# Optimization experiments

Hardware: AMD Instinct MI355X
Metric: run time of the kernel (lower is better)

Reference implementation:

```python
import jax, jax.numpy as jnp
from jax import lax
import numpy as np

S, B, T, N, FJ, H, MF, M = 8, 64, 64, 16, 32, 128, 16, 8
NN = S + M  # total machine-graph nodes
EPS = 1e-5
SLOPE = 0.2


def layernorm(x, g, b):
    mu = x.mean(-1, keepdims=True)
    var = ((x - mu) ** 2).mean(-1, keepdims=True)
    return (x - mu) / jnp.sqrt(var + EPS) * g + b


def gat(adj, x, W, a):
    # dense GAT layer: x [..., N, Fin], adj [..., N, N]
    h = x @ W  # [..., N, O]
    O = W.shape[1]
    f1 = h @ a[:O]  # [..., N]
    f2 = h @ a[O:]
    e = jax.nn.leaky_relu(f1[..., :, None] + f2[..., None, :], SLOPE)
    e = jnp.where(adj > 0, e, jnp.float32(-1e9))
    return jax.nn.softmax(e, axis=-1) @ h


def job_enc(adj, x, Ws, As):
    t = jnp.tanh(gat(adj, x, Ws[0], As[0]))
    t = jnp.tanh(gat(adj, t, Ws[1], As[1]) + t)
    t = jnp.tanh(gat(adj, t, Ws[2], As[2]) + t)
    t = jnp.tanh(t + gat(adj, t, Ws[3], As[3]))
    return t.mean(-2)  # mean over ops dim


def lstm_last(x, Wih, Whh, b):
    # x: [Bx, T, H]; returns final hidden state [Bx, H]
    xs = jnp.einsum('bti,gi->tbg', x, Wih) + b  # [T, Bx, 4H]
    h0 = jnp.zeros((x.shape[0], Whh.shape[1]), x.dtype)

    def step(carry, xt):
        h, c = carry
        g = xt + h @ Whh.T
        i, f, gg, o = jnp.split(g, 4, axis=-1)
        c = jax.nn.sigmoid(f) * c + jax.nn.sigmoid(i) * jnp.tanh(gg)
        h = jax.nn.sigmoid(o) * jnp.tanh(c)
        return (h, c), None

    (h, _), _ = lax.scan(step, (h0, h0), xs)
    return h


def setup_inputs() -> dict:
    key = jax.random.key(0)
    ks = jax.random.split(key, 32)

    def adj(k, shape):
        a = jax.random.bernoulli(k, 0.4, shape).astype(jnp.int32)
        return jnp.maximum(a, jnp.eye(shape[-1], dtype=jnp.int32))

    mfeat = jax.random.normal(ks[4], (B, NN, MF), jnp.float32)
    # stage nodes (first S) have feature[...,0] > 0; machine nodes < 0
    mfeat = mfeat.at[:, :S, 0].set(jnp.abs(mfeat[:, :S, 0]) + 0.1)
    mfeat = mfeat.at[:, S:, 0].set(-jnp.abs(mfeat[:, S:, 0]) - 0.1)

    sc = 0.08
    inp = {
        'j_stages_f': jax.random.normal(ks[0], (S, B, T, N, FJ), jnp.float32),
        'j_stages_a': adj(ks[1], (S, B, T, N, N)),
        'j_machine_f': jax.random.normal(ks[2], (B, M, N, FJ), jnp.float32),
        'j_machine_a': adj(ks[3], (B, M, N, N)),
        'machine_f': mfeat,
        'machine_a': adj(ks[5], (B, NN, NN)),
        'jg1_W': jax.random.normal(ks[6], (FJ, H), jnp.float32) * sc,
        'jgW': jax.random.normal(ks[7], (3, H, H), jnp.float32) * sc,
        'jga': jax.random.normal(ks[8], (4, 2 * H), jnp.float32) * sc,
        'lstm_Wih': jax.random.normal(ks[9], (4 * H, H), jnp.float32) * sc,
        'lstm_Whh': jax.random.normal(ks[10], (4 * H, H), jnp.float32) * sc,
        'lstm_b': jnp.zeros((4 * H,), jnp.float32),
        'mfe_W': jax.random.normal(ks[11], (MF, H), jnp.float32) * sc,
        'mfe_b': jnp.zeros((H,), jnp.float32),
        'n2_g': jnp.ones((H,), jnp.float32),
        'n2_b': jnp.zeros((H,), jnp.float32),
        'me_W': jax.random.normal(ks[12], (2 * H, H), jnp.float32) * sc,
        'me_b': jnp.zeros((H,), jnp.float32),
        'n3_g': jnp.ones((H,), jnp.float32),
        'n3_b': jnp.zeros((H,), jnp.float32),
        'mgW': jax.random.normal(ks[13], (4, H, H), jnp.float32) * sc,
        'mga': jax.random.normal(ks[14], (4, 2 * H), jnp.float32) * sc,
        'mng': jnp.ones((4, H), jnp.float32),
        'mnb': jnp.zeros((4, H), jnp.float32),
    }
    return inp


def reference(j_stages_f, j_stages_a, j_machine_f, j_machine_a, machine_f,
              machine_a, jg1_W, jgW, jga, lstm_Wih, lstm_Whh, lstm_b,
              mfe_W, mfe_b, n2_g, n2_b, me_W, me_b, n3_g, n3_b,
              mgW, mga, mng, mnb):
    Ws = [jg1_W, jgW[0], jgW[1], jgW[2]]
    As = [jga[0], jga[1], jga[2], jga[3]]

    # per-stage job encoding + LSTM over job sequence
    stage_emb = jax.vmap(lambda a, f: job_enc(a, f, Ws, As))(j_stages_a, j_stages_f)  # [S,B,T,H]
    hlast = lstm_last(stage_emb.reshape(S * B, T, H), lstm_Wih, lstm_Whh, lstm_b)
    j_encoded = hlast.reshape(S, B, H).transpose(1, 0, 2)  # [B,S,H]

    # machine-side job graph encoding (shared encoder)
    jm = job_enc(j_machine_a, j_machine_f, Ws, As)  # [B,M,H]

    # machine node embedding
    mfh = jnp.tanh(layernorm(machine_f @ mfe_W + mfe_b, n2_g, n2_b))  # [B,NN,H]

    # static routing: first S nodes -> stage contexts, rest -> machine contexts
    ctx = jnp.concatenate([j_encoded, jm], axis=1)  # [B,NN,H]
    nodes = jnp.concatenate([mfh, ctx], axis=-1)  # [B,NN,2H]
    nodes = jnp.tanh(layernorm(nodes @ me_W + me_b, n3_g, n3_b))

    h = nodes
    prev = None
    for k in range(4):
        h2 = layernorm(gat(machine_a, h, mgW[k], mga[k]), mng[k], mnb[k])
        if k != 0:
            h2 = h2 + prev
        h = jnp.tanh(h2)
        prev = h
    return h.mean(axis=1)  # [B, H]
```

## Files before the change

kernel.cpp:

```cpp
#include <hip/hip_runtime.h>
#include <hip/hip_bf16.h>
#include <math.h>

#define S_ 8
#define B_ 64
#define T_ 64
#define N_ 16
#define FJ_ 32
#define H_ 128
#define MF_ 16
#define M_ 8
#define SB_ 512
#define G1_ 32768
#define G2_ 512

#define CPAD 132
#define PPAD 17

typedef short bf16x8 __attribute__((ext_vector_type(8)));
typedef short bf16x4 __attribute__((ext_vector_type(4)));
typedef float f32x4 __attribute__((ext_vector_type(4)));
typedef unsigned short u16;

__device__ __forceinline__ u16 f2bf(float f) {
  union { float f; unsigned u; } v; v.f = f;
  unsigned r = v.u + 0x7FFFu + ((v.u >> 16) & 1u);
  return (u16)(r >> 16);
}
__device__ __forceinline__ unsigned pk2(float lo, float hi) {
  __hip_bfloat162 h2 = __float22bfloat162_rn(make_float2(lo, hi));
  union { __hip_bfloat162 h; unsigned u; } x; x.h = h2; return x.u;
}
__device__ __forceinline__ bf16x4 mkfrag(unsigned a, unsigned b) {
  union { bf16x4 v; unsigned u[2]; } x; x.u[0] = a; x.u[1] = b; return x.v;
}
__device__ __forceinline__ f32x4 mfma16(bf16x4 a, bf16x4 b, f32x4 c) {
#if __has_builtin(__builtin_amdgcn_mfma_f32_16x16x16bf16_1k)
  return __builtin_amdgcn_mfma_f32_16x16x16bf16_1k(a, b, c, 0, 0, 0);
#else
  asm("v_mfma_f32_16x16x16_bf16 %0, %1, %2, %0" : "+v"(c) : "v"(a), "v"(b));
  return c;
#endif
}
__device__ __forceinline__ float frcp(float x) {
#if __has_builtin(__builtin_amdgcn_rcpf)
  return __builtin_amdgcn_rcpf(x);
#else
  return 1.f / x;
#endif
}
__device__ __forceinline__ float frsq(float x) {
#if __has_builtin(__builtin_amdgcn_rsqf)
  return __builtin_amdgcn_rsqf(x);
#else
  return rsqrtf(x);
#endif
}
__device__ __forceinline__ float ftanh(float x) {
  float e = __expf(2.f * x);
  return fmaf(-2.f, frcp(e + 1.f), 1.f);
}
__device__ __forceinline__ float sigmoidf_(float x) {
  return frcp(1.f + __expf(-x));
}

__device__ __forceinline__ void fma8(float (&acc)[8], float xv, float4 wa, float4 wb) {
  acc[0] = fmaf(xv, wa.x, acc[0]); acc[1] = fmaf(xv, wa.y, acc[1]);
  acc[2] = fmaf(xv, wa.z, acc[2]); acc[3] = fmaf(xv, wa.w, acc[3]);
  acc[4] = fmaf(xv, wb.x, acc[4]); acc[5] = fmaf(xv, wb.y, acc[5]);
  acc[6] = fmaf(xv, wb.z, acc[6]); acc[7] = fmaf(xv, wb.w, acc[7]);
}
__device__ __forceinline__ float grp16_sum(float v) {
#pragma unroll
  for (int m = 1; m < 16; m <<= 1) v += __shfl_xor(v, m);
  return v;
}
__device__ __forceinline__ float grp16_max(float v) {
#pragma unroll
  for (int m = 1; m < 16; m <<= 1) v = fmaxf(v, __shfl_xor(v, m));
  return v;
}
__device__ __forceinline__ void ln_row(float (&v)[8], const float* gw, const float* bw, int j0) {
  float s1 = 0.f, s2 = 0.f;
#pragma unroll
  for (int c = 0; c < 8; ++c) { s1 += v[c]; s2 += v[c] * v[c]; }
  s1 = grp16_sum(s1); s2 = grp16_sum(s2);
  float mu = s1 * (1.f / 128.f);
  float var = s2 * (1.f / 128.f) - mu * mu;
  float rstd = frsq(var + 1e-5f);
#pragma unroll
  for (int c = 0; c < 8; ++c) v[c] = (v[c] - mu) * rstd * gw[j0 + c] + bw[j0 + c];
}

__global__ __launch_bounds__(256) void pack_w_kernel(
    const float* __restrict__ W0, const float* __restrict__ W123,
    const float* __restrict__ jga,
    const float* __restrict__ Wih, const float* __restrict__ Whh,
    u16* __restrict__ wpk0, u16* __restrict__ wpkL,
    u16* __restrict__ wpkIH, u16* __restrict__ wpkHH)
{
  int idx = blockIdx.x * 256 + threadIdx.x;
  if (idx < 4608) {
    int e = idx & 3, l = (idx >> 2) & 63, t = idx >> 8;
    int n = t >> 1, kk = t & 1;
    int q = l >> 4, cc = l & 15;
    int k = 16 * kk + 4 * q + e;
    float v = 0.f;
    if (n < 8) v = W0[k * 128 + 16 * n + cc];
    else if (cc < 2) {
      const float* a = jga + cc * 128;
      float s = 0.f;
      for (int j = 0; j < 128; ++j) s += W0[k * 128 + j] * a[j];
      v = s;
    }
    wpk0[idx] = f2bf(v);
  } else if (idx < 59904) {
    int id = idx - 4608;
    int e = id & 3, l = (id >> 2) & 63;
    int t2 = id >> 8;
    int t = t2 % 72, layer = t2 / 72;
    int n = t >> 3, kk = t & 7;
    int q = l >> 4, cc = l & 15;
    int k = 16 * kk + 4 * q + e;
    const float* W = W123 + (size_t)layer * 16384;
    float v = 0.f;
    if (n < 8) v = W[k * 128 + 16 * n + cc];
    else if (cc < 2) {
      const float* a = jga + (layer + 1) * 256 + cc * 128;
      float s = 0.f;
      for (int j = 0; j < 128; ++j) s += W[k * 128 + j] * a[j];
      v = s;
    }
    wpkL[id] = f2bf(v);
  } else if (idx < 125440) {
    int id = idx - 59904;
    int e = id & 7, l = (id >> 3) & 63, kk = (id >> 9) & 3, n = id >> 11;
    int gate = 16 * n + (l & 15), k = 32 * kk + 8 * (l >> 4) + e;
    wpkIH[id] = f2bf(Wih[gate * 128 + k]);
  } else if (idx < 190976) {
    int id = idx - 125440;
    int e = id & 7, l = (id >> 3) & 63, kk = (id >> 9) & 3, n = id >> 11;
    int gate = 16 * n + (l & 15), k = 32 * kk + 8 * (l >> 4) + e;
    wpkHH[id] = f2bf(Whh[gate * 128 + k]);
  }
}

__global__ __launch_bounds__(512) __attribute__((amdgpu_waves_per_eu(2, 4)))
void gat_mfma_kernel(
    const float* __restrict__ xinA,
    const int* __restrict__ adjA,
    float* __restrict__ outmA, u16* __restrict__ outbfA,
    const float* __restrict__ xinB,
    const int* __restrict__ adjB,
    float* __restrict__ outmB, u16* __restrict__ outbfB,
    const u16* __restrict__ wpk0, const u16* __restrict__ wpkL)
{
  __shared__ __align__(16) u16 wbuf[18432];
  __shared__ __align__(16) float fbuf[8][32];

  const int wv = threadIdx.x >> 6;
  const int l = threadIdx.x & 63;
  const int c = l & 15, q = l >> 4;
  float* fb = fbuf[wv];

  const float* xin; const int* adjin; float* outm; u16* outbf; int g;
  if (blockIdx.x < G1_ / 8) {
    xin = xinA; adjin = adjA; outm = outmA; outbf = outbfA;
    g = blockIdx.x * 8 + wv;
  } else {
    xin = xinB; adjin = adjB; outm = outmB; outbf = outbfB;
    g = (blockIdx.x - G1_ / 8) * 8 + wv;
  }

  auto stage = [&](const u16* src, int nbytes) {
    const float4* s4 = (const float4*)src;
    float4* d4 = (float4*)wbuf;
    int n16 = nbytes >> 4;
    for (int i = threadIdx.x; i < n16; i += 512) d4[i] = s4[i];
  };

  int4 A1 = *(const int4*)(adjin + (size_t)g * 256 + c * 16 + 4 * q);

  f32x4 res[8];
  bf16x4 hfrag[8];

  auto softmax_pv = [&](f32x4 Cf, bool resid) {
    if (c < 2) *(f32x4*)(fb + c * 16 + 4 * q) = Cf;
    float f1v = fb[c];
    float4 f2v = *(const float4*)(fb + 16 + 4 * q);
    float ev[4] = {f1v + f2v.x, f1v + f2v.y, f1v + f2v.z, f1v + f2v.w};
#pragma unroll
    for (int e = 0; e < 4; ++e) ev[e] = (ev[e] >= 0.f) ? ev[e] : 0.2f * ev[e];
    ev[0] = (A1.x > 0) ? ev[0] : -1e9f;
    ev[1] = (A1.y > 0) ? ev[1] : -1e9f;
    ev[2] = (A1.z > 0) ? ev[2] : -1e9f;
    ev[3] = (A1.w > 0) ? ev[3] : -1e9f;
    float mx = fmaxf(fmaxf(ev[0], ev[1]), fmaxf(ev[2], ev[3]));
    mx = fmaxf(mx, __shfl_xor(mx, 16));
    mx = fmaxf(mx, __shfl_xor(mx, 32));
    float sm = 0.f;
#pragma unroll
    for (int e = 0; e < 4; ++e) { ev[e] = __expf(ev[e] - mx); sm += ev[e]; }
    sm += __shfl_xor(sm, 16);
    sm += __shfl_xor(sm, 32);
    float zinv = frcp(sm);
    bf16x4 pfrag = mkfrag(pk2(ev[0] * zinv, ev[1] * zinv), pk2(ev[2] * zinv, ev[3] * zinv));
#pragma unroll
    for (int m = 0; m < 8; ++m) {
      f32x4 o = resid ? res[m] : (f32x4){0.f, 0.f, 0.f, 0.f};
      o = mfma16(hfrag[m], pfrag, o);
      f32x4 t;
      t[0] = ftanh(o[0]); t[1] = ftanh(o[1]); t[2] = ftanh(o[2]); t[3] = ftanh(o[3]);
      res[m] = t;
    }
  };

  stage(wpk0, 9216);
  __syncthreads();
  {
    bf16x4 xf[2];
    const float* xg = xin + (size_t)g * 512 + c * 32 + 4 * q;
    float4 x1 = *(const float4*)xg;
    float4 x2 = *(const float4*)(xg + 16);
    xf[0] = mkfrag(pk2(x1.x, x1.y), pk2(x1.z, x1.w));
    xf[1] = mkfrag(pk2(x2.x, x2.y), pk2(x2.z, x2.w));
#pragma unroll
    for (int n = 0; n < 8; ++n) {
      f32x4 Ch = (f32x4){0.f, 0.f, 0.f, 0.f};
#pragma unroll
      for (int kk = 0; kk < 2; ++kk) {
        bf16x4 wf = *(const bf16x4*)(wbuf + ((n * 2 + kk) * 64 + l) * 4);
        Ch = mfma16(xf[kk], wf, Ch);
      }
      hfrag[n] = mkfrag(pk2(Ch[0], Ch[1]), pk2(Ch[2], Ch[3]));
    }
    f32x4 Cf = (f32x4){0.f, 0.f, 0.f, 0.f};
#pragma unroll
    for (int kk = 0; kk < 2; ++kk) {
      bf16x4 wf = *(const bf16x4*)(wbuf + ((16 + kk) * 64 + l) * 4);
      Cf = mfma16(xf[kk], wf, Cf);
    }
    softmax_pv(Cf, false);
  }
  __syncthreads();

#pragma unroll 1
  for (int layer = 1; layer < 4; ++layer) {
    stage(wpkL + (size_t)(layer - 1) * 18432, 36864);
    __syncthreads();
    bf16x4 xf[8];
#pragma unroll
    for (int kk = 0; kk < 8; ++kk)
      xf[kk] = mkfrag(pk2(res[kk][0], res[kk][1]), pk2(res[kk][2], res[kk][3]));
#pragma unroll
    for (int n = 0; n < 8; ++n) {
      f32x4 Ch = (f32x4){0.f, 0.f, 0.f, 0.f};
#pragma unroll
      for (int kk = 0; kk < 8; ++kk) {
        bf16x4 wf = *(const bf16x4*)(wbuf + ((n * 8 + kk) * 64 + l) * 4);
        Ch = mfma16(xf[kk], wf, Ch);
      }
      hfrag[n] = mkfrag(pk2(Ch[0], Ch[1]), pk2(Ch[2], Ch[3]));
    }
    f32x4 Cf = (f32x4){0.f, 0.f, 0.f, 0.f};
#pragma unroll
    for (int kk = 0; kk < 8; ++kk) {
      bf16x4 wf = *(const bf16x4*)(wbuf + ((64 + kk) * 64 + l) * 4);
      Cf = mfma16(xf[kk], wf, Cf);
    }
    softmax_pv(Cf, true);
    __syncthreads();
  }

  u16* tb = wbuf + wv * 2176;
#pragma unroll
  for (int m = 0; m < 8; ++m) {
    uint2 u;
    u.x = pk2(res[m][0], res[m][1]);
    u.y = pk2(res[m][2], res[m][3]);
    *(uint2*)(tb + c * 136 + 16 * m + 4 * q) = u;
  }
  {
    float s0 = 0.f, s1 = 0.f;
#pragma unroll
    for (int node = 0; node < 16; ++node) {
      unsigned u = *(const unsigned*)(tb + node * 136 + 2 * l);
      union { unsigned u; float f; } lo, hi;
      lo.u = u << 16; hi.u = u & 0xffff0000u;
      s0 += lo.f; s1 += hi.f;
    }
    s0 *= 0.0625f; s1 *= 0.0625f;
    *(float2*)(outm + (size_t)g * 128 + 2 * l) = make_float2(s0, s1);
    *(unsigned*)(outbf + (size_t)g * 128 + 2 * l) = pk2(s0, s1);
  }
}

__global__ __launch_bounds__(512) __attribute__((amdgpu_waves_per_eu(1, 2)))
void lstm_fused_kernel(
    const u16* __restrict__ emb_bf,
    const u16* __restrict__ wpkIH, const u16* __restrict__ wpkHH,
    const float* __restrict__ bvec,
    float* __restrict__ hlast)
{
  __shared__ unsigned hbuf[2][1024];
  const int tid = threadIdx.x;
  const int w = tid >> 6, l = tid & 63;
  const int c = l & 15, q = l >> 4;
  const int seq0 = blockIdx.x * 16;
  const int swz = (c & 7) << 2;

  bf16x8 aih[4][4], ahh[4][4];
#pragma unroll
  for (int m = 0; m < 4; ++m)
#pragma unroll
    for (int kk = 0; kk < 4; ++kk) {
      int n = 8 * m + w;
      aih[m][kk] = *(const bf16x8*)(wpkIH + ((size_t)((n * 4 + kk) * 64 + l)) * 8);
      ahh[m][kk] = *(const bf16x8*)(wpkHH + ((size_t)((n * 4 + kk) * 64 + l)) * 8);
    }
  float bias[4][4];
#pragma unroll
  for (int m = 0; m < 4; ++m)
#pragma unroll
    for (int r = 0; r < 4; ++r) bias[m][r] = bvec[128 * m + 16 * w + 4 * q + r];

  hbuf[0][tid] = 0u;
  hbuf[0][512 + tid] = 0u;
  __syncthreads();

  const u16* xbase = emb_bf + ((size_t)(seq0 + c)) * 64 * 128 + q * 8;

  f32x4 accih[4];
  {
    bf16x8 xf[4];
#pragma unroll
    for (int kk = 0; kk < 4; ++kk) xf[kk] = *(const bf16x8*)(xbase + kk * 32);
#pragma unroll
    for (int m = 0; m < 4; ++m) {
      f32x4 a = (f32x4){0.f, 0.f, 0.f, 0.f};
#pragma unroll
      for (int kk = 0; kk < 4; ++kk)
        a = __builtin_amdgcn_mfma_f32_16x16x32_bf16(aih[m][kk], xf[kk], a, 0, 0, 0);
      accih[m] = a;
    }
  }

  float cst[4] = {0.f, 0.f, 0.f, 0.f};
  float hv[4] = {0.f, 0.f, 0.f, 0.f};
  int pb = 0;
#pragma unroll 1
  for (int t = 0; t < T_; ++t) {
    bf16x8 hf[4];
#pragma unroll
    for (int kk = 0; kk < 4; ++kk) {
      int j0 = (16 * kk + 4 * q) ^ swz;
      hf[kk] = *(const bf16x8*)&hbuf[pb][c * 64 + j0];
    }
    f32x4 acc[4];
#pragma unroll
    for (int m = 0; m < 4; ++m) {
      f32x4 a = accih[m];
#pragma unroll
      for (int kk = 0; kk < 4; ++kk)
        a = __builtin_amdgcn_mfma_f32_16x16x32_bf16(ahh[m][kk], hf[kk], a, 0, 0, 0);
      acc[m] = a;
    }
#pragma unroll
    for (int r = 0; r < 4; ++r) {
      float ig = acc[0][r] + bias[0][r];
      float fg = acc[1][r] + bias[1][r];
      float gg = acc[2][r] + bias[2][r];
      float og = acc[3][r] + bias[3][r];
      cst[r] = sigmoidf_(fg) * cst[r] + sigmoidf_(ig) * ftanh(gg);
      hv[r] = sigmoidf_(og) * ftanh(cst[r]);
    }
    {
      int j0 = (8 * w + 2 * q) ^ swz;
      uint2 u2; u2.x = pk2(hv[0], hv[1]); u2.y = pk2(hv[2], hv[3]);
      *(uint2*)&hbuf[pb ^ 1][c * 64 + j0] = u2;
    }
    __syncthreads();
    pb ^= 1;
    if (t < T_ - 1) {
      bf16x8 xf[4];
      const u16* xr = xbase + (t + 1) * 128;
#pragma unroll
      for (int kk = 0; kk < 4; ++kk) xf[kk] = *(const bf16x8*)(xr + kk * 32);
#pragma unroll
      for (int m = 0; m < 4; ++m) {
        f32x4 a = (f32x4){0.f, 0.f, 0.f, 0.f};
#pragma unroll
        for (int kk = 0; kk < 4; ++kk)
          a = __builtin_amdgcn_mfma_f32_16x16x32_bf16(aih[m][kk], xf[kk], a, 0, 0, 0);
        accih[m] = a;
      }
    }
  }
#pragma unroll
  for (int r = 0; r < 4; ++r)
    hlast[((size_t)(seq0 + c)) * 128 + 16 * w + 4 * q + r] = hv[r];
}

__global__ __launch_bounds__(256) __attribute__((amdgpu_waves_per_eu(2, 4)))
void machine_kernel(
    const float* __restrict__ machine_f, const int* __restrict__ machine_a,
    const float* __restrict__ hlast, const float* __restrict__ jm,
    const float* __restrict__ mfe_W, const float* __restrict__ mfe_b,
    const float* __restrict__ n2_g, const float* __restrict__ n2_b,
    const float* __restrict__ me_W, const float* __restrict__ me_b,
    const float* __restrict__ n3_g, const float* __restrict__ n3_b,
    const float* __restrict__ mgW, const float* __restrict__ mga,
    const float* __restrict__ mng, const float* __restrict__ mnb,
    float* __restrict__ outp)
{
  __shared__ float mf[256];
  __shared__ int adjs[256];
  __shared__ __align__(16) float ctx[16 * CPAD];
  __shared__ __align__(16) float mfh[16 * CPAD];
  __shared__ __align__(16) float cur[16 * CPAD];
  __shared__ __align__(16) float tmp[16 * CPAD];
  __shared__ __align__(16) float prevb[16 * CPAD];
  __shared__ float pm[16 * PPAD];
  __shared__ float f1s[16], f2s[16];

  const int b = blockIdx.x;
  const int tid = threadIdx.x;
  const int i = tid >> 4;
  const int jb = tid & 15;
  const int j0 = jb << 3;

  mf[tid] = machine_f[(size_t)b * 256 + tid];
  adjs[tid] = machine_a[(size_t)b * 256 + tid];
  {
    const float* src = (i < 8) ? (hlast + ((size_t)i * B_ + b) * H_)
                               : (jm + ((size_t)b * M_ + (i - 8)) * H_);
    *(float4*)(ctx + i * CPAD + j0) = ((const float4*)src)[jb * 2];
    *(float4*)(ctx + i * CPAD + j0 + 4) = ((const float4*)src)[jb * 2 + 1];
  }
  __syncthreads();

  {
    float acc[8];
#pragma unroll
    for (int c = 0; c < 8; ++c) acc[c] = 0.f;
#pragma unroll
    for (int k = 0; k < MF_; ++k) {
      float xv = mf[i * 16 + k];
      float4 wa = *(const float4*)(mfe_W + (size_t)k * H_ + j0);
      float4 wb = *(const float4*)(mfe_W + (size_t)k * H_ + j0 + 4);
      fma8(acc, xv, wa, wb);
    }
#pragma unroll
    for (int c = 0; c < 8; ++c) acc[c] += mfe_b[j0 + c];
    ln_row(acc, n2_g, n2_b, j0);
#pragma unroll
    for (int c = 0; c < 8; ++c) mfh[i * CPAD + j0 + c] = ftanh(acc[c]);
  }
  __syncthreads();

  {
    float acc[8];
#pragma unroll
    for (int c = 0; c < 8; ++c) acc[c] = 0.f;
#pragma unroll 4
    for (int k = 0; k < H_; ++k) {
      float xv = mfh[i * CPAD + k];
      float4 wa = *(const float4*)(me_W + (size_t)k * H_ + j0);
      float4 wb = *(const float4*)(me_W + (size_t)k * H_ + j0 + 4);
      fma8(acc, xv, wa, wb);
    }
#pragma unroll 4
    for (int k = 0; k < H_; ++k) {
      float xv = ctx[i * CPAD + k];
      float4 wa = *(const float4*)(me_W + (size_t)(128 + k) * H_ + j0);
      float4 wb = *(const float4*)(me_W + (size_t)(128 + k) * H_ + j0 + 4);
      fma8(acc, xv, wa, wb);
    }
#pragma unroll
    for (int c = 0; c < 8; ++c) acc[c] += me_b[j0 + c];
    ln_row(acc, n3_g, n3_b, j0);
#pragma unroll
    for (int c = 0; c < 8; ++c) cur[i * CPAD + j0 + c] = ftanh(acc[c]);
  }
  __syncthreads();

  for (int l = 0; l < 4; ++l) {
    const float* W = mgW + (size_t)l * H_ * H_;
    const float* a0 = mga + l * 256;
    const float* a1 = a0 + 128;

    float acc[8];
#pragma unroll
    for (int c = 0; c < 8; ++c) acc[c] = 0.f;
#pragma unroll 4
    for (int k = 0; k < H_; ++k) {
      float xv = cur[i * CPAD + k];
      float4 wa = *(const float4*)(W + (size_t)k * H_ + j0);
      float4 wb = *(const float4*)(W + (size_t)k * H_ + j0 + 4);
      fma8(acc, xv, wa, wb);
    }
    *(float4*)(tmp + i * CPAD + j0) = make_float4(acc[0], acc[1], acc[2], acc[3]);
    *(float4*)(tmp + i * CPAD + j0 + 4) = make_float4(acc[4], acc[5], acc[6], acc[7]);

    float p1 = 0.f, p2 = 0.f;
#pragma unroll
    for (int c = 0; c < 8; ++c) {
      p1 = fmaf(acc[c], a0[j0 + c], p1);
      p2 = fmaf(acc[c], a1[j0 + c], p2);
    }
    p1 = grp16_sum(p1); p2 = grp16_sum(p2);
    if (jb == 0) { f1s[i] = p1; f2s[i] = p2; }
    __syncthreads();

    {
      int jc = jb;
      float e = f1s[i] + f2s[jc];
      e = (e >= 0.f) ? e : 0.2f * e;
      if (adjs[i * 16 + jc] <= 0) e = -1e9f;
      float mxv = grp16_max(e);
      float ex = __expf(e - mxv);
      float smv = grp16_sum(ex);
      pm[i * PPAD + jc] = ex * frcp(smv);
    }
    __syncthreads();

    float o[8];
#pragma unroll
    for (int c = 0; c < 8; ++c) o[c] = 0.f;
#pragma unroll
    for (int k = 0; k < 16; ++k) {
      float pv = pm[i * PPAD + k];
      float4 ha = *(const float4*)(tmp + k * CPAD + j0);
      float4 hb = *(const float4*)(tmp + k * CPAD + j0 + 4);
      fma8(o, pv, ha, hb);
    }
    ln_row(o, mng + l * H_, mnb + l * H_, j0);
#pragma unroll
    for (int c = 0; c < 8; ++c) {
      float v = o[c] + ((l > 0) ? prevb[i * CPAD + j0 + c] : 0.f);
      v = ftanh(v);
      cur[i * CPAD + j0 + c] = v;
      prevb[i * CPAD + j0 + c] = v;
    }
    __syncthreads();
  }

  if (tid < 128) {
    float s = 0.f;
#pragma unroll
    for (int r = 0; r < 16; ++r) s += cur[r * CPAD + tid];
    outp[(size_t)b * H_ + tid] = s * (1.f / 16.f);
  }
}

extern "C" void kernel_launch(void* const* d_in, const int* in_sizes, int n_in,
                              void* d_out, int out_size, void* d_ws, size_t ws_size,
                              hipStream_t stream) {
  const float* j_stages_f  = (const float*)d_in[0];
  const int*   j_stages_a  = (const int*)d_in[1];
  const float* j_machine_f = (const float*)d_in[2];
  const int*   j_machine_a = (const int*)d_in[3];
  const float* machine_f   = (const float*)d_in[4];
  const int*   machine_a   = (const int*)d_in[5];
  const float* jg1_W       = (const float*)d_in[6];
  const float* jgW         = (const float*)d_in[7];
  const float* jga         = (const float*)d_in[8];
  const float* lstm_Wih    = (const float*)d_in[9];
  const float* lstm_Whh    = (const float*)d_in[10];
  const float* lstm_b      = (const float*)d_in[11];
  const float* mfe_W       = (const float*)d_in[12];
  const float* mfe_b       = (const float*)d_in[13];
  const float* n2_g        = (const float*)d_in[14];
  const float* n2_b        = (const float*)d_in[15];
  const float* me_W        = (const float*)d_in[16];
  const float* me_b        = (const float*)d_in[17];
  const float* n3_g        = (const float*)d_in[18];
  const float* n3_b        = (const float*)d_in[19];
  const float* mgW         = (const float*)d_in[20];
  const float* mga         = (const float*)d_in[21];
  const float* mng         = (const float*)d_in[22];
  const float* mnb         = (const float*)d_in[23];
  float* out = (float*)d_out;

  char* ws = (char*)d_ws;
  u16*   emb_bf  = (u16*)ws;
  u16*   jmbf    = (u16*)(ws + 8388608);
  float* jm      = (float*)(ws + 8519680);
  float* hlast   = (float*)(ws + 8781824);
  float* outm_s  = (float*)(ws + 9043968);
  u16*   wpk0    = (u16*)(ws + 25821184);
  u16*   wpkL    = (u16*)(ws + 25830400);
  u16*   wpkIH   = (u16*)(ws + 25940992);
  u16*   wpkHH   = (u16*)(ws + 26072064);

  pack_w_kernel<<<746, 256, 0, stream>>>(jg1_W, jgW, jga, lstm_Wih, lstm_Whh,
                                         wpk0, wpkL, wpkIH, wpkHH);
  gat_mfma_kernel<<<G1_ / 8 + G2_ / 8, 512, 0, stream>>>(
      j_stages_f, j_stages_a, outm_s, emb_bf,
      j_machine_f, j_machine_a, jm, jmbf, wpk0, wpkL);
  lstm_fused_kernel<<<SB_ / 16, 512, 0, stream>>>(emb_bf, wpkIH, wpkHH, lstm_b, hlast);
  machine_kernel<<<B_, 256, 0, stream>>>(machine_f, machine_a, hlast, jm,
                                         mfe_W, mfe_b, n2_g, n2_b, me_W, me_b,
                                         n3_g, n3_b, mgW, mga, mng, mnb, out);
}
```

Before: 368.6 us.

## Use 16x16x32 MFMA in GAT, halve LSTM sequences per block, prefetch inputs

The GAT kernel moves from 16x16x16 bf16 MFMA to 16x16x32 MFMA. The weight packing is rebuilt to match, and the fragments are reshuffled with cross-lane shuffles, including zero-padding the attention matrix for the K=16 P·V product. The unused float stage output write is dropped. The LSTM kernel now handles 8 sequences per block instead of 16, doubling the block count, and computes the next step's input projection before the barrier while prefetching the input two steps ahead. These changes aim to use fewer MFMA instructions and to add parallelism and latency hiding to the serial LSTM. The cost is extra shuffles and wasted half tiles in the LSTM MFMAs.

```diff
diff --git a/kernel.cpp b/kernel.cpp
--- a/kernel.cpp
+++ b/kernel.cpp
@@ -18,7 +18,6 @@
 #define PPAD 17
 
 typedef short bf16x8 __attribute__((ext_vector_type(8)));
-typedef short bf16x4 __attribute__((ext_vector_type(4)));
 typedef float f32x4 __attribute__((ext_vector_type(4)));
 typedef unsigned short u16;
 
@@ -31,16 +30,12 @@
   __hip_bfloat162 h2 = __float22bfloat162_rn(make_float2(lo, hi));
   union { __hip_bfloat162 h; unsigned u; } x; x.h = h2; return x.u;
 }
-__device__ __forceinline__ bf16x4 mkfrag(unsigned a, unsigned b) {
-  union { bf16x4 v; unsigned u[2]; } x; x.u[0] = a; x.u[1] = b; return x.v;
-}
-__device__ __forceinline__ f32x4 mfma16(bf16x4 a, bf16x4 b, f32x4 c) {
-#if __has_builtin(__builtin_amdgcn_mfma_f32_16x16x16bf16_1k)
-  return __builtin_amdgcn_mfma_f32_16x16x16bf16_1k(a, b, c, 0, 0, 0);
-#else
-  asm("v_mfma_f32_16x16x16_bf16 %0, %1, %2, %0" : "+v"(c) : "v"(a), "v"(b));
-  return c;
-#endif
+__device__ __forceinline__ bf16x8 mk8(unsigned a, unsigned b, unsigned cc, unsigned d) {
+  union { bf16x8 v; unsigned u[4]; } x;
+  x.u[0] = a; x.u[1] = b; x.u[2] = cc; x.u[3] = d; return x.v;
+}
+__device__ __forceinline__ f32x4 mfma32(bf16x8 a, bf16x8 b, f32x4 c) {
+  return __builtin_amdgcn_mfma_f32_16x16x32_bf16(a, b, c, 0, 0, 0);
 }
 __device__ __forceinline__ float frcp(float x) {
 #if __has_builtin(__builtin_amdgcn_rcpf)
@@ -101,10 +96,9 @@
 {
   int idx = blockIdx.x * 256 + threadIdx.x;
   if (idx < 4608) {
-    int e = idx & 3, l = (idx >> 2) & 63, t = idx >> 8;
-    int n = t >> 1, kk = t & 1;
+    int e = idx & 7, l = (idx >> 3) & 63, n = idx >> 9;
     int q = l >> 4, cc = l & 15;
-    int k = 16 * kk + 4 * q + e;
+    int k = 8 * q + e;
     float v = 0.f;
     if (n < 8) v = W0[k * 128 + 16 * n + cc];
     else if (cc < 2) {
@@ -116,12 +110,12 @@
     wpk0[idx] = f2bf(v);
   } else if (idx < 59904) {
     int id = idx - 4608;
-    int e = id & 3, l = (id >> 2) & 63;
-    int t2 = id >> 8;
-    int t = t2 % 72, layer = t2 / 72;
-    int n = t >> 3, kk = t & 7;
+    int e = id & 7, l = (id >> 3) & 63;
+    int t2 = id >> 9;
+    int t = t2 % 36, layer = t2 / 36;
+    int n = t >> 2, kk = t & 3;
     int q = l >> 4, cc = l & 15;
-    int k = 16 * kk + 4 * q + e;
+    int k = 32 * kk + 8 * q + e;
     const float* W = W123 + (size_t)layer * 16384;
     float v = 0.f;
     if (n < 8) v = W[k * 128 + 16 * n + cc];
@@ -147,11 +141,9 @@
 
 __global__ __launch_bounds__(512) __attribute__((amdgpu_waves_per_eu(2, 4)))
 void gat_mfma_kernel(
-    const float* __restrict__ xinA,
-    const int* __restrict__ adjA,
+    const float* __restrict__ xinA, const int* __restrict__ adjA,
     float* __restrict__ outmA, u16* __restrict__ outbfA,
-    const float* __restrict__ xinB,
-    const int* __restrict__ adjB,
+    const float* __restrict__ xinB, const int* __restrict__ adjB,
     float* __restrict__ outmB, u16* __restrict__ outbfB,
     const u16* __restrict__ wpk0, const u16* __restrict__ wpkL)
 {
@@ -182,7 +174,12 @@
   int4 A1 = *(const int4*)(adjin + (size_t)g * 256 + c * 16 + 4 * q);
 
   f32x4 res[8];
-  bf16x4 hfrag[8];
+  unsigned hp0[8], hp1[8];
+  const int sLo = c + 16 * (2 * q);
+  const int sHi = sLo + 16;
+  const int sA = c + 16 * (2 * (q & 1));
+  const int sB = sA + 16;
+  const bool qhi = (q >= 2);
 
   auto softmax_pv = [&](f32x4 Cf, bool resid) {
     if (c < 2) *(f32x4*)(fb + c * 16 + 4 * q) = Cf;
@@ -204,42 +201,39 @@
     sm += __shfl_xor(sm, 16);
     sm += __shfl_xor(sm, 32);
     float zinv = frcp(sm);
-    bf16x4 pfrag = mkfrag(pk2(ev[0] * zinv, ev[1] * zinv), pk2(ev[2] * zinv, ev[3] * zinv));
-#pragma unroll
-    for (int m = 0; m < 8; ++m) {
-      f32x4 o = resid ? res[m] : (f32x4){0.f, 0.f, 0.f, 0.f};
-      o = mfma16(hfrag[m], pfrag, o);
+    unsigned pp0 = pk2(ev[0] * zinv, ev[1] * zinv);
+    unsigned pp1 = pk2(ev[2] * zinv, ev[3] * zinv);
+    unsigned w0 = __shfl(pp0, sLo), w1 = __shfl(pp1, sLo);
+    unsigned w2 = __shfl(pp0, sHi), w3 = __shfl(pp1, sHi);
+    if (qhi) { w0 = 0u; w1 = 0u; w2 = 0u; w3 = 0u; }
+    bf16x8 pfrag = mk8(w0, w1, w2, w3);
+#pragma unroll
+    for (int n = 0; n < 8; ++n) {
+      unsigned v0 = __shfl(hp0[n], sLo), v1 = __shfl(hp1[n], sLo);
+      unsigned v2 = __shfl(hp0[n], sHi), v3 = __shfl(hp1[n], sHi);
+      f32x4 o = resid ? res[n] : (f32x4){0.f, 0.f, 0.f, 0.f};
+      o = mfma32(mk8(v0, v1, v2, v3), pfrag, o);
       f32x4 t;
       t[0] = ftanh(o[0]); t[1] = ftanh(o[1]); t[2] = ftanh(o[2]); t[3] = ftanh(o[3]);
-      res[m] = t;
+      res[n] = t;
     }
   };
 
   stage(wpk0, 9216);
   __syncthreads();
   {
-    bf16x4 xf[2];
-    const float* xg = xin + (size_t)g * 512 + c * 32 + 4 * q;
+    const float* xg = xin + (size_t)g * 512 + c * 32 + q * 8;
     float4 x1 = *(const float4*)xg;
-    float4 x2 = *(const float4*)(xg + 16);
-    xf[0] = mkfrag(pk2(x1.x, x1.y), pk2(x1.z, x1.w));
-    xf[1] = mkfrag(pk2(x2.x, x2.y), pk2(x2.z, x2.w));
+    float4 x2 = *(const float4*)(xg + 4);
+    bf16x8 xf8 = mk8(pk2(x1.x, x1.y), pk2(x1.z, x1.w), pk2(x2.x, x2.y), pk2(x2.z, x2.w));
 #pragma unroll
     for (int n = 0; n < 8; ++n) {
       f32x4 Ch = (f32x4){0.f, 0.f, 0.f, 0.f};
-#pragma unroll
-      for (int kk = 0; kk < 2; ++kk) {
-        bf16x4 wf = *(const bf16x4*)(wbuf + ((n * 2 + kk) * 64 + l) * 4);
-        Ch = mfma16(xf[kk], wf, Ch);
-      }
-      hfrag[n] = mkfrag(pk2(Ch[0], Ch[1]), pk2(Ch[2], Ch[3]));
+      Ch = mfma32(xf8, *(const bf16x8*)(wbuf + (n * 64 + l) * 8), Ch);
+      hp0[n] = pk2(Ch[0], Ch[1]); hp1[n] = pk2(Ch[2], Ch[3]);
     }
     f32x4 Cf = (f32x4){0.f, 0.f, 0.f, 0.f};
-#pragma unroll
-    for (int kk = 0; kk < 2; ++kk) {
-      bf16x4 wf = *(const bf16x4*)(wbuf + ((16 + kk) * 64 + l) * 4);
-      Cf = mfma16(xf[kk], wf, Cf);
-    }
+    Cf = mfma32(xf8, *(const bf16x8*)(wbuf + (8 * 64 + l) * 8), Cf);
     softmax_pv(Cf, false);
   }
   __syncthreads();
@@ -248,26 +242,33 @@
   for (int layer = 1; layer < 4; ++layer) {
     stage(wpkL + (size_t)(layer - 1) * 18432, 36864);
     __syncthreads();
-    bf16x4 xf[8];
-#pragma unroll
-    for (int kk = 0; kk < 8; ++kk)
-      xf[kk] = mkfrag(pk2(res[kk][0], res[kk][1]), pk2(res[kk][2], res[kk][3]));
+    unsigned p0[8], p1[8];
+#pragma unroll
+    for (int m = 0; m < 8; ++m) {
+      p0[m] = pk2(res[m][0], res[m][1]);
+      p1[m] = pk2(res[m][2], res[m][3]);
+    }
+    bf16x8 xf[4];
+#pragma unroll
+    for (int kk = 0; kk < 4; ++kk) {
+      unsigned a0 = __shfl(p0[2 * kk], sA), b0 = __shfl(p0[2 * kk + 1], sA);
+      unsigned a1 = __shfl(p1[2 * kk], sA), b1 = __shfl(p1[2 * kk + 1], sA);
+      unsigned a2 = __shfl(p0[2 * kk], sB), b2 = __shfl(p0[2 * kk + 1], sB);
+      unsigned a3 = __shfl(p1[2 * kk], sB), b3 = __shfl(p1[2 * kk + 1], sB);
+      xf[kk] = mk8(qhi ? b0 : a0, qhi ? b1 : a1, qhi ? b2 : a2, qhi ? b3 : a3);
+    }
 #pragma unroll
     for (int n = 0; n < 8; ++n) {
       f32x4 Ch = (f32x4){0.f, 0.f, 0.f, 0.f};
 #pragma unroll
-      for (int kk = 0; kk < 8; ++kk) {
-        bf16x4 wf = *(const bf16x4*)(wbuf + ((n * 8 + kk) * 64 + l) * 4);
-        Ch = mfma16(xf[kk], wf, Ch);
-      }
-      hfrag[n] = mkfrag(pk2(Ch[0], Ch[1]), pk2(Ch[2], Ch[3]));
+      for (int kk = 0; kk < 4; ++kk)
+        Ch = mfma32(xf[kk], *(const bf16x8*)(wbuf + ((n * 4 + kk) * 64 + l) * 8), Ch);
+      hp0[n] = pk2(Ch[0], Ch[1]); hp1[n] = pk2(Ch[2], Ch[3]);
     }
     f32x4 Cf = (f32x4){0.f, 0.f, 0.f, 0.f};
 #pragma unroll
-    for (int kk = 0; kk < 8; ++kk) {
-      bf16x4 wf = *(const bf16x4*)(wbuf + ((64 + kk) * 64 + l) * 4);
-      Cf = mfma16(xf[kk], wf, Cf);
-    }
+    for (int kk = 0; kk < 4; ++kk)
+      Cf = mfma32(xf[kk], *(const bf16x8*)(wbuf + ((32 + kk) * 64 + l) * 8), Cf);
     softmax_pv(Cf, true);
     __syncthreads();
   }
@@ -290,7 +291,7 @@
       s0 += lo.f; s1 += hi.f;
     }
     s0 *= 0.0625f; s1 *= 0.0625f;
-    *(float2*)(outm + (size_t)g * 128 + 2 * l) = make_float2(s0, s1);
+    if (outm) *(float2*)(outm + (size_t)g * 128 + 2 * l) = make_float2(s0, s1);
     *(unsigned*)(outbf + (size_t)g * 128 + 2 * l) = pk2(s0, s1);
   }
 }
@@ -306,7 +307,8 @@
   const int tid = threadIdx.x;
   const int w = tid >> 6, l = tid & 63;
   const int c = l & 15, q = l >> 4;
-  const int seq0 = blockIdx.x * 16;
+  const int ce = c & 7;
+  const int seq0 = blockIdx.x * 8;
   const int swz = (c & 7) << 2;
 
   bf16x8 aih[4][4], ahh[4][4];
@@ -328,8 +330,9 @@
   hbuf[0][512 + tid] = 0u;
   __syncthreads();
 
-  const u16* xbase = emb_bf + ((size_t)(seq0 + c)) * 64 * 128 + q * 8;
-
+  const u16* xbase = emb_bf + ((size_t)(seq0 + ce)) * 64 * 128 + q * 8;
+
+  bf16x8 xnxt[4];
   f32x4 accih[4];
   {
     bf16x8 xf[4];
@@ -343,6 +346,8 @@
         a = __builtin_amdgcn_mfma_f32_16x16x32_bf16(aih[m][kk], xf[kk], a, 0, 0, 0);
       accih[m] = a;
     }
+#pragma unroll
+    for (int kk = 0; kk < 4; ++kk) xnxt[kk] = *(const bf16x8*)(xbase + 128 + kk * 32);
   }
 
   float cst[4] = {0.f, 0.f, 0.f, 0.f};
@@ -379,26 +384,29 @@
       uint2 u2; u2.x = pk2(hv[0], hv[1]); u2.y = pk2(hv[2], hv[3]);
       *(uint2*)&hbuf[pb ^ 1][c * 64 + j0] = u2;
     }
+    if (t < T_ - 1) {
+#pragma unroll
+      for (int m = 0; m < 4; ++m) {
+        f32x4 a = (f32x4){0.f, 0.f, 0.f, 0.f};
+#pragma unroll
+        for (int kk = 0; kk < 4; ++kk)
+          a = __builtin_amdgcn_mfma_f32_16x16x32_bf16(aih[m][kk], xnxt[kk], a, 0, 0, 0);
+        accih[m] = a;
+      }
+      if (t < T_ - 2) {
+        const u16* xr = xbase + (size_t)(t + 2) * 128;
+#pragma unroll
+        for (int kk = 0; kk < 4; ++kk) xnxt[kk] = *(const bf16x8*)(xr + kk * 32);
+      }
+    }
     __syncthreads();
     pb ^= 1;
-    if (t < T_ - 1) {
-      bf16x8 xf[4];
-      const u16* xr = xbase + (t + 1) * 128;
-#pragma unroll
-      for (int kk = 0; kk < 4; ++kk) xf[kk] = *(const bf16x8*)(xr + kk * 32);
-#pragma unroll
-      for (int m = 0; m < 4; ++m) {
-        f32x4 a = (f32x4){0.f, 0.f, 0.f, 0.f};
-#pragma unroll
-        for (int kk = 0; kk < 4; ++kk)
-          a = __builtin_amdgcn_mfma_f32_16x16x32_bf16(aih[m][kk], xf[kk], a, 0, 0, 0);
-        accih[m] = a;
-      }
-    }
-  }
-#pragma unroll
-  for (int r = 0; r < 4; ++r)
-    hlast[((size_t)(seq0 + c)) * 128 + 16 * w + 4 * q + r] = hv[r];
+  }
+  if (c < 8) {
+#pragma unroll
+    for (int r = 0; r < 4; ++r)
+      hlast[((size_t)(seq0 + ce)) * 128 + 16 * w + 4 * q + r] = hv[r];
+  }
 }
 
 __global__ __launch_bounds__(256) __attribute__((amdgpu_waves_per_eu(2, 4)))
@@ -484,9 +492,9 @@
   }
   __syncthreads();
 
-  for (int l = 0; l < 4; ++l) {
-    const float* W = mgW + (size_t)l * H_ * H_;
-    const float* a0 = mga + l * 256;
+  for (int ll = 0; ll < 4; ++ll) {
+    const float* W = mgW + (size_t)ll * H_ * H_;
+    const float* a0 = mga + ll * 256;
     const float* a1 = a0 + 128;
 
     float acc[8];
@@ -534,10 +542,10 @@
       float4 hb = *(const float4*)(tmp + k * CPAD + j0 + 4);
       fma8(o, pv, ha, hb);
     }
-    ln_row(o, mng + l * H_, mnb + l * H_, j0);
+    ln_row(o, mng + ll * H_, mnb + ll * H_, j0);
 #pragma unroll
     for (int c = 0; c < 8; ++c) {
-      float v = o[c] + ((l > 0) ? prevb[i * CPAD + j0 + c] : 0.f);
+      float v = o[c] + ((ll > 0) ? prevb[i * CPAD + j0 + c] : 0.f);
       v = ftanh(v);
       cur[i * CPAD + j0 + c] = v;
       prevb[i * CPAD + j0 + c] = v;
@@ -587,18 +595,17 @@
   u16*   jmbf    = (u16*)(ws + 8388608);
   float* jm      = (float*)(ws + 8519680);
   float* hlast   = (float*)(ws + 8781824);
-  float* outm_s  = (float*)(ws + 9043968);
-  u16*   wpk0    = (u16*)(ws + 25821184);
-  u16*   wpkL    = (u16*)(ws + 25830400);
-  u16*   wpkIH   = (u16*)(ws + 25940992);
-  u16*   wpkHH   = (u16*)(ws + 26072064);
+  u16*   wpk0    = (u16*)(ws + 9043968);
+  u16*   wpkL    = (u16*)(ws + 9053184);
+  u16*   wpkIH   = (u16*)(ws + 9163776);
+  u16*   wpkHH   = (u16*)(ws + 9294848);
 
   pack_w_kernel<<<746, 256, 0, stream>>>(jg1_W, jgW, jga, lstm_Wih, lstm_Whh,
                                          wpk0, wpkL, wpkIH, wpkHH);
   gat_mfma_kernel<<<G1_ / 8 + G2_ / 8, 512, 0, stream>>>(
-      j_stages_f, j_stages_a, outm_s, emb_bf,
+      j_stages_f, j_stages_a, (float*)nullptr, emb_bf,
       j_machine_f, j_machine_a, jm, jmbf, wpk0, wpkL);
-  lstm_fused_kernel<<<SB_ / 16, 512, 0, stream>>>(emb_bf, wpkIH, wpkHH, lstm_b, hlast);
+  lstm_fused_kernel<<<SB_ / 8, 512, 0, stream>>>(emb_bf, wpkIH, wpkHH, lstm_b, hlast);
   machine_kernel<<<B_, 256, 0, stream>>>(machine_f, machine_a, hlast, jm,
                                          mfe_W, mfe_b, n2_g, n2_b, me_W, me_b,
                                          n3_g, n3_b, mgW, mga, mng, mnb, out);
```

After: 349.4 us. -5.2%, faster.
